# Performance work log

Hardware: AMD Instinct MI355X
Metric: run time of the kernel (lower is better)

## Reference

```python
import jax, jax.numpy as jnp
import numpy as np

H = 12          # num attention heads
D_HEAD = 64     # head size (768 / 12)
P = 2           # power-law exponent
C = 5.0         # score shift
EPS = 1e-10


def setup_inputs() -> dict:
    key = jax.random.key(0)
    ks = jax.random.split(key, 8)
    B, S, Dm = 32, 512, 768
    scale = 1.0 / np.sqrt(Dm)
    return {
        "hidden_states": jax.random.normal(ks[0], (B, S, Dm), dtype=jnp.float32),
        "attention_mask": jnp.ones((B, 1, 1, S), dtype=jnp.float32),
        "Wq": jax.random.normal(ks[1], (Dm, Dm), dtype=jnp.float32) * scale,
        "bq": jnp.zeros((Dm,), dtype=jnp.float32),
        "Wk": jax.random.normal(ks[2], (Dm, Dm), dtype=jnp.float32) * scale,
        "bk": jnp.zeros((Dm,), dtype=jnp.float32),
        "Wv": jax.random.normal(ks[3], (Dm, Dm), dtype=jnp.float32) * scale,
        "bv": jnp.zeros((Dm,), dtype=jnp.float32),
    }


def _heads(x, B, S):
    # [B, S, H*d] -> [B, H, S, d]
    return x.reshape(B, S, H, D_HEAD).transpose(0, 2, 1, 3)


def reference(hidden_states, attention_mask, Wq, bq, Wk, bk, Wv, bv):
    B, S, Dm = hidden_states.shape
    q = _heads(hidden_states @ Wq + bq, B, S)
    k = _heads(hidden_states @ Wk + bk, B, S)
    v = _heads(hidden_states @ Wv + bv, B, S)

    inv_sqrt_d = 1.0 / (np.sqrt(D_HEAD) + 1e-10)
    scores = jnp.einsum("bhqd,bhkd->bhqk", q, k) * inv_sqrt_d  # [B,H,S,S]

    # Power-law attention (Powerformer, distill=0 branch)
    probs = jnp.power(scores + C, P)
    probs = probs / (jnp.sum(probs, axis=-1, keepdims=True) + EPS)
    probs = probs * attention_mask  # mask multiplied after normalization

    ctx = jnp.einsum("bhqk,bhkd->bhqd", probs, v)  # [B,H,S,d]
    ctx = ctx.transpose(0, 2, 1, 3).reshape(B, S, Dm)
    return ctx
```

## Files before the change

kernel.cpp:

```cpp
#include <hip/hip_runtime.h>

typedef __attribute__((ext_vector_type(8))) _Float16 half8;
typedef __attribute__((ext_vector_type(4))) _Float16 half4;
typedef __attribute__((ext_vector_type(4))) float f32x4;

#define MFMA_K32(a, b, c) __builtin_amdgcn_mfma_f32_16x16x32_f16((a), (b), (c), 0, 0, 0)
#define MFMA_K16(a, b, c) __builtin_amdgcn_mfma_f32_16x16x16f16((a), (b), (c), 0, 0, 0)

__device__ inline void async16(const _Float16* g, _Float16* l) {
    __builtin_amdgcn_global_load_lds(
        (const __attribute__((address_space(1))) void*)g,
        (__attribute__((address_space(3))) void*)l, 16, 0, 0);
}


__global__ __launch_bounds__(256) void prep_kernel(
    const float* __restrict__ X, _Float16* __restrict__ Xh,
    const float* __restrict__ W0, const float* __restrict__ W1,
    const float* __restrict__ W2,
    _Float16* __restrict__ T0, _Float16* __restrict__ T1,
    _Float16* __restrict__ T2)
{
    __shared__ float tile[32][33];
    int bid = blockIdx.x;
    if (bid < 6144) {
        size_t idx = ((size_t)bid * 256 + threadIdx.x) * 8;
        float4 a = *(const float4*)(X + idx);
        float4 c = *(const float4*)(X + idx + 4);
        half8 hv;
        hv[0] = (_Float16)a.x; hv[1] = (_Float16)a.y;
        hv[2] = (_Float16)a.z; hv[3] = (_Float16)a.w;
        hv[4] = (_Float16)c.x; hv[5] = (_Float16)c.y;
        hv[6] = (_Float16)c.z; hv[7] = (_Float16)c.w;
        *(half8*)(Xh + idx) = hv;
    } else {
        int id = bid - 6144;
        int z = id / 576; id -= z * 576;
        int n0 = (id / 24) * 32, k0 = (id % 24) * 32;
        const float* W = (z == 0) ? W0 : (z == 1) ? W1 : W2;
        _Float16* T = (z == 0) ? T0 : (z == 1) ? T1 : T2;
        int tx = threadIdx.x & 31, ty = threadIdx.x >> 5;
#pragma unroll
        for (int r = 0; r < 4; ++r)
            tile[ty + 8 * r][tx] = W[(size_t)(k0 + ty + 8 * r) * 768 + n0 + tx];
        __syncthreads();
#pragma unroll
        for (int r = 0; r < 4; ++r)
            T[(size_t)(n0 + ty + 8 * r) * 768 + k0 + tx] =
                (_Float16)tile[tx][ty + 8 * r];
    }
}

__global__ __launch_bounds__(256) void qkv_gemm(
    const _Float16* __restrict__ Xh,
    const _Float16* __restrict__ W0, const _Float16* __restrict__ W1,
    const _Float16* __restrict__ W2,
    const float* __restrict__ b0, const float* __restrict__ b1,
    const float* __restrict__ b2,
    const float* __restrict__ mask,
    _Float16* __restrict__ Qo, _Float16* __restrict__ Ko,
    _Float16* __restrict__ Vo)
{
    int z = blockIdx.y / 6;
    int n0 = (blockIdx.y % 6) * 128;
    int m0 = blockIdx.x * 128;
    const _Float16* Wt = (z == 0) ? W0 : (z == 1) ? W1 : W2;
    const float* bias = (z == 0) ? b0 : (z == 1) ? b1 : b2;

    __shared__ __attribute__((aligned(16))) _Float16 As[2 * 8192];
    __shared__ __attribute__((aligned(16))) _Float16 Bs[2 * 8192];

    int t = threadIdx.x;
    int wave = t >> 6, lane = t & 63, quad = lane >> 4, l16 = lane & 15;
    int wm = (wave & 1) * 64, wn = (wave >> 1) * 64;

    int srow = t >> 3;
    int sg = (t & 7) ^ (srow & 7);

    const _Float16* gA = Xh + (size_t)(m0 + srow) * 768 + sg * 8;
    const _Float16* gB = Wt + (size_t)(n0 + srow) * 768 + sg * 8;
    _Float16* lA = As + t * 8;
    _Float16* lB = Bs + t * 8;

#define STAGE(buf, k0v) do {                                                   \
        async16(gA,                    lA + (buf) * 8192);                     \
        async16(gA + (size_t)1 * 32 * 768 + (k0v) - (k0v) + (k0v), lA + (buf) * 8192 + 2048); \
        async16(gA + (size_t)2 * 32 * 768 + (k0v), lA + (buf) * 8192 + 4096);  \
        async16(gA + (size_t)3 * 32 * 768 + (k0v), lA + (buf) * 8192 + 6144);  \
        async16(gB + (k0v),            lB + (buf) * 8192);                     \
        async16(gB + (size_t)1 * 32 * 768 + (k0v), lB + (buf) * 8192 + 2048);  \
        async16(gB + (size_t)2 * 32 * 768 + (k0v), lB + (buf) * 8192 + 4096);  \
        async16(gB + (size_t)3 * 32 * 768 + (k0v), lB + (buf) * 8192 + 6144); } while (0)
#undef STAGE
#define STAGE(buf, k0v) do {                                                   \
        async16(gA + (k0v),                        lA + (buf) * 8192);         \
        async16(gA + (size_t)1 * 32 * 768 + (k0v), lA + (buf) * 8192 + 2048);  \
        async16(gA + (size_t)2 * 32 * 768 + (k0v), lA + (buf) * 8192 + 4096);  \
        async16(gA + (size_t)3 * 32 * 768 + (k0v), lA + (buf) * 8192 + 6144);  \
        async16(gB + (k0v),                        lB + (buf) * 8192);         \
        async16(gB + (size_t)1 * 32 * 768 + (k0v), lB + (buf) * 8192 + 2048);  \
        async16(gB + (size_t)2 * 32 * 768 + (k0v), lB + (buf) * 8192 + 4096);  \
        async16(gB + (size_t)3 * 32 * 768 + (k0v), lB + (buf) * 8192 + 6144); } while (0)

    const _Float16* Pa = (z == 2) ? As : Bs;
    const _Float16* Pb = (z == 2) ? Bs : As;

    f32x4 acc[4][4] = {};

    STAGE(0, 0);

    for (int kt = 0; kt < 12; ++kt) {
        int c = kt & 1;
        if (kt < 11) {
            STAGE(c ^ 1, (kt + 1) * 64);
            asm volatile("s_waitcnt vmcnt(8)" ::: "memory");
        } else {
            asm volatile("s_waitcnt vmcnt(0)" ::: "memory");
        }
        __builtin_amdgcn_s_barrier();
        __builtin_amdgcn_sched_barrier(0);

        const _Float16* Pa_ = Pa + c * 8192;
        const _Float16* Pb_ = Pb + c * 8192;
#pragma unroll
        for (int ks = 0; ks < 2; ++ks) {
            half8 af[4], bf[4];
#pragma unroll
            for (int i = 0; i < 4; ++i) {
                int row = wm + i * 16 + l16;
                af[i] = *(const half8*)&Pa_[row * 64 +
                                            (((ks << 2) + quad) ^ (row & 7)) * 8];
            }
#pragma unroll
            for (int j = 0; j < 4; ++j) {
                int row = wn + j * 16 + l16;
                bf[j] = *(const half8*)&Pb_[row * 64 +
                                            (((ks << 2) + quad) ^ (row & 7)) * 8];
            }
#pragma unroll
            for (int i = 0; i < 4; ++i)
#pragma unroll
                for (int j = 0; j < 4; ++j)
                    acc[i][j] = MFMA_K32(af[i], bf[j], acc[i][j]);
        }
        __builtin_amdgcn_sched_barrier(0);
        __builtin_amdgcn_s_barrier();
    }
#undef STAGE

    if (z != 2) {
#pragma unroll
        for (int i = 0; i < 4; ++i) {
            int nbase = n0 + wm + i * 16 + quad * 4;
            int hh = nbase >> 6, dbase = nbase & 63;
            float4 bv4 = *(const float4*)&bias[nbase];
#pragma unroll
            for (int j = 0; j < 4; ++j) {
                int token = m0 + wn + j * 16 + l16;
                int bb = token >> 9, s = token & 511;
                half4 pk;
                if (z == 0) {
#pragma unroll
                    for (int r = 0; r < 4; ++r)
                        pk[r] = (_Float16)((acc[i][j][r] + ((const float*)&bv4)[r]) * 0.125f);
                } else {
#pragma unroll
                    for (int r = 0; r < 4; ++r)
                        pk[r] = (_Float16)(acc[i][j][r] + ((const float*)&bv4)[r]);
                }
                size_t off = (((size_t)(bb * 12 + hh)) * 512 + s) * 64 + dbase;
                if (z == 0) *(half4*)&Qo[off] = pk;
                else        *(half4*)&Ko[off] = pk;
            }
        }
    } else {
        float mk[4][4];
#pragma unroll
        for (int i = 0; i < 4; ++i) {
            int mbase = m0 + wm + i * 16 + quad * 4;
            int bb = mbase >> 9, s = mbase & 511;
#pragma unroll
            for (int r = 0; r < 4; ++r)
                mk[i][r] = mask[(size_t)bb * 512 + s + r];
        }
#pragma unroll
        for (int j = 0; j < 4; ++j) {
            int n = n0 + wn + j * 16 + l16;
            float bv = bias[n];
            int hh = n >> 6, d = n & 63;
#pragma unroll
            for (int i = 0; i < 4; ++i) {
                int mbase = m0 + wm + i * 16 + quad * 4;
                int bb = mbase >> 9, s = mbase & 511;
                half4 pk;
#pragma unroll
                for (int r = 0; r < 4; ++r)
                    pk[r] = (_Float16)((acc[i][j][r] + bv) * mk[i][r]);
                size_t off = (((size_t)(bb * 12 + hh)) * 64 + d) * 512 + s;
                *(half4*)&Vo[off] = pk;
            }
        }
    }
}

__global__ __launch_bounds__(256) void attn_kernel(
    const _Float16* __restrict__ Q, const _Float16* __restrict__ K,
    const _Float16* __restrict__ Vt, float* __restrict__ out)
{
    __shared__ __attribute__((aligned(16))) _Float16 Ks[2][64 * 88];
    __shared__ __attribute__((aligned(16))) _Float16 Vs[2][64 * 88];

    int t = threadIdx.x;
    int wave = t >> 6, lane = t & 63, quad = lane >> 4, l16 = lane & 15;
    int h = blockIdx.y, b = blockIdx.z;
    size_t bh = (size_t)b * 12 + h;
    const _Float16* Qp = Q + bh * (512 * 64);
    const _Float16* Kp = K + bh * (512 * 64);
    const _Float16* Vp = Vt + bh * (64 * 512);
    int qbase = blockIdx.x * 256 + wave * 64;

    half8 qf[4][2];
#pragma unroll
    for (int i = 0; i < 4; ++i)
#pragma unroll
        for (int ks = 0; ks < 2; ++ks)
            qf[i][ks] = *(const half8*)(Qp + (size_t)(qbase + i * 16 + l16) * 64 +
                                        ks * 32 + quad * 8);

    f32x4 ctx[4][4] = {};
    f32x4 rsum[4] = {};
    const half4 ones = {(_Float16)1.f, (_Float16)1.f, (_Float16)1.f, (_Float16)1.f};

    int srow = t >> 2, spart = (t & 3) * 16;
    const _Float16* kgb = Kp + (size_t)srow * 64 + spart;
    const _Float16* vgb = Vp + (size_t)srow * 512 + spart;

    half8 ka0 = *(const half8*)(kgb);
    half8 ka1 = *(const half8*)(kgb + 8);
    half8 va0 = *(const half8*)(vgb);
    half8 va1 = *(const half8*)(vgb + 8);
    *(half8*)&Ks[0][srow * 88 + spart] = ka0;
    *(half8*)&Ks[0][srow * 88 + spart + 8] = ka1;
    *(half8*)&Vs[0][srow * 88 + spart] = va0;
    *(half8*)&Vs[0][srow * 88 + spart + 8] = va1;
    __syncthreads();

    for (int kt = 0; kt < 8; ++kt) {
        int c = kt & 1;
        if (kt < 7) {
            size_t ko = (size_t)(kt + 1) * 64;
            ka0 = *(const half8*)(kgb + ko * 64);
            ka1 = *(const half8*)(kgb + ko * 64 + 8);
            va0 = *(const half8*)(vgb + ko);
            va1 = *(const half8*)(vgb + ko + 8);
        }

        __builtin_amdgcn_s_setprio(1);
#pragma unroll
        for (int kb = 0; kb < 4; ++kb) {
            half8 kf0 = *(const half8*)&Ks[c][(kb * 16 + l16) * 88 + quad * 8];
            half8 kf1 = *(const half8*)&Ks[c][(kb * 16 + l16) * 88 + 32 + quad * 8];
            f32x4 sc[4];
#pragma unroll
            for (int i = 0; i < 4; ++i) {
                f32x4 s0 = {0.f, 0.f, 0.f, 0.f};
                s0 = MFMA_K32(kf0, qf[i][0], s0);
                sc[i] = MFMA_K32(kf1, qf[i][1], s0);
            }
            half4 pA[4];
#pragma unroll
            for (int i = 0; i < 4; ++i) {
#pragma unroll
                for (int r = 0; r < 4; ++r) {
                    float s = sc[i][r] + 5.0f;
                    pA[i][r] = (_Float16)(s * s);
                }
            }
#pragma unroll
            for (int i = 0; i < 4; ++i)
                rsum[i] = MFMA_K16(pA[i], ones, rsum[i]);
#pragma unroll
            for (int n = 0; n < 4; ++n) {
                half4 vf = *(const half4*)&Vs[c][(n * 16 + l16) * 88 + kb * 16 + quad * 4];
#pragma unroll
                for (int i = 0; i < 4; ++i)
                    ctx[i][n] = MFMA_K16(pA[i], vf, ctx[i][n]);
            }
        }
        __builtin_amdgcn_s_setprio(0);

        if (kt < 7) {
            *(half8*)&Ks[1 - c][srow * 88 + spart] = ka0;
            *(half8*)&Ks[1 - c][srow * 88 + spart + 8] = ka1;
            *(half8*)&Vs[1 - c][srow * 88 + spart] = va0;
            *(half8*)&Vs[1 - c][srow * 88 + spart + 8] = va1;
        }
        __syncthreads();
    }

#pragma unroll
    for (int i = 0; i < 4; ++i) {
        f32x4 inv;
#pragma unroll
        for (int r = 0; r < 4; ++r)
            inv[r] = 1.0f / (rsum[i][r] + 1e-10f);
#pragma unroll
        for (int n = 0; n < 4; ++n)
#pragma unroll
            for (int r = 0; r < 4; ++r) {
                int q = qbase + i * 16 + quad * 4 + r;
                int d = n * 16 + l16;
                out[((size_t)b * 512 + q) * 768 + h * 64 + d] =
                    ctx[i][n][r] * inv[r];
            }
    }
}

extern "C" void kernel_launch(void* const* d_in, const int* in_sizes, int n_in,
                              void* d_out, int out_size, void* d_ws, size_t ws_size,
                              hipStream_t stream)
{
    const float* hs   = (const float*)d_in[0];
    const float* mask = (const float*)d_in[1];
    const float* Wq   = (const float*)d_in[2];
    const float* bq   = (const float*)d_in[3];
    const float* Wk   = (const float*)d_in[4];
    const float* bk   = (const float*)d_in[5];
    const float* Wv   = (const float*)d_in[6];
    const float* bv   = (const float*)d_in[7];
    float* out = (float*)d_out;

    char* ws = (char*)d_ws;
    _Float16* Wtq = (_Float16*)ws;
    _Float16* Wtk = Wtq + 768 * 768;
    _Float16* Wtv = Wtk + 768 * 768;
    _Float16* Qb  = Wtv + 768 * 768;
    _Float16* Kb  = Qb + 16384 * 768;
    _Float16* Vb  = Kb + 16384 * 768;
    _Float16* Xh = (_Float16*)d_out;

    prep_kernel<<<dim3(7872), 256, 0, stream>>>(hs, Xh, Wq, Wk, Wv,
                                                Wtq, Wtk, Wtv);
    qkv_gemm<<<dim3(128, 18), 256, 0, stream>>>(Xh, Wtq, Wtk, Wtv,
                                                bq, bk, bv, mask, Qb, Kb, Vb);
    attn_kernel<<<dim3(2, 12, 32), 256, 0, stream>>>(Qb, Kb, Vb, out);
}
```

Baseline: 239.5 us.

## Fuse fp32-to-fp16 activation cast into QKV GEMM A-tile loads

Removes the separate pass that converted hidden_states to fp16 in global memory. The QKV GEMM now loads fp32 activation tiles into registers, converts them, and writes fp16 into LDS, prefetching one k-step ahead. The fp16 weight transpose/cast kernel remains. The change avoids a full write and re-read of the fp16 activation copy. In exchange each GEMM block reads twice the A bytes from global memory, and the 18 column blocks that share a row tile each redo the same conversion. It also adds register pressure and synchronous LDS stores in place of async global-to-LDS copies.

```diff
diff --git a/kernel.cpp b/kernel.cpp
--- a/kernel.cpp
+++ b/kernel.cpp
@@ -14,45 +14,30 @@
 }
 
 
-__global__ __launch_bounds__(256) void prep_kernel(
-    const float* __restrict__ X, _Float16* __restrict__ Xh,
+__global__ __launch_bounds__(256) void wcast_kernel(
     const float* __restrict__ W0, const float* __restrict__ W1,
     const float* __restrict__ W2,
     _Float16* __restrict__ T0, _Float16* __restrict__ T1,
     _Float16* __restrict__ T2)
 {
+    int z = blockIdx.z;
+    const float* W = (z == 0) ? W0 : (z == 1) ? W1 : W2;
+    _Float16* T = (z == 0) ? T0 : (z == 1) ? T1 : T2;
     __shared__ float tile[32][33];
-    int bid = blockIdx.x;
-    if (bid < 6144) {
-        size_t idx = ((size_t)bid * 256 + threadIdx.x) * 8;
-        float4 a = *(const float4*)(X + idx);
-        float4 c = *(const float4*)(X + idx + 4);
-        half8 hv;
-        hv[0] = (_Float16)a.x; hv[1] = (_Float16)a.y;
-        hv[2] = (_Float16)a.z; hv[3] = (_Float16)a.w;
-        hv[4] = (_Float16)c.x; hv[5] = (_Float16)c.y;
-        hv[6] = (_Float16)c.z; hv[7] = (_Float16)c.w;
-        *(half8*)(Xh + idx) = hv;
-    } else {
-        int id = bid - 6144;
-        int z = id / 576; id -= z * 576;
-        int n0 = (id / 24) * 32, k0 = (id % 24) * 32;
-        const float* W = (z == 0) ? W0 : (z == 1) ? W1 : W2;
-        _Float16* T = (z == 0) ? T0 : (z == 1) ? T1 : T2;
-        int tx = threadIdx.x & 31, ty = threadIdx.x >> 5;
-#pragma unroll
-        for (int r = 0; r < 4; ++r)
-            tile[ty + 8 * r][tx] = W[(size_t)(k0 + ty + 8 * r) * 768 + n0 + tx];
-        __syncthreads();
-#pragma unroll
-        for (int r = 0; r < 4; ++r)
-            T[(size_t)(n0 + ty + 8 * r) * 768 + k0 + tx] =
-                (_Float16)tile[tx][ty + 8 * r];
-    }
+    int n0 = blockIdx.x * 32, k0 = blockIdx.y * 32;
+    int tx = threadIdx.x & 31, ty = threadIdx.x >> 5;
+#pragma unroll
+    for (int r = 0; r < 4; ++r)
+        tile[ty + 8 * r][tx] = W[(size_t)(k0 + ty + 8 * r) * 768 + n0 + tx];
+    __syncthreads();
+#pragma unroll
+    for (int r = 0; r < 4; ++r)
+        T[(size_t)(n0 + ty + 8 * r) * 768 + k0 + tx] =
+            (_Float16)tile[tx][ty + 8 * r];
 }
 
 __global__ __launch_bounds__(256) void qkv_gemm(
-    const _Float16* __restrict__ Xh,
+    const float* __restrict__ X,
     const _Float16* __restrict__ W0, const _Float16* __restrict__ W1,
     const _Float16* __restrict__ W2,
     const float* __restrict__ b0, const float* __restrict__ b1,
@@ -77,43 +62,52 @@
     int srow = t >> 3;
     int sg = (t & 7) ^ (srow & 7);
 
-    const _Float16* gA = Xh + (size_t)(m0 + srow) * 768 + sg * 8;
+    const float*    gX = X  + (size_t)(m0 + srow) * 768 + sg * 8;
     const _Float16* gB = Wt + (size_t)(n0 + srow) * 768 + sg * 8;
     _Float16* lA = As + t * 8;
     _Float16* lB = Bs + t * 8;
 
-#define STAGE(buf, k0v) do {                                                   \
-        async16(gA,                    lA + (buf) * 8192);                     \
-        async16(gA + (size_t)1 * 32 * 768 + (k0v) - (k0v) + (k0v), lA + (buf) * 8192 + 2048); \
-        async16(gA + (size_t)2 * 32 * 768 + (k0v), lA + (buf) * 8192 + 4096);  \
-        async16(gA + (size_t)3 * 32 * 768 + (k0v), lA + (buf) * 8192 + 6144);  \
-        async16(gB + (k0v),            lB + (buf) * 8192);                     \
-        async16(gB + (size_t)1 * 32 * 768 + (k0v), lB + (buf) * 8192 + 2048);  \
-        async16(gB + (size_t)2 * 32 * 768 + (k0v), lB + (buf) * 8192 + 4096);  \
-        async16(gB + (size_t)3 * 32 * 768 + (k0v), lB + (buf) * 8192 + 6144); } while (0)
-#undef STAGE
-#define STAGE(buf, k0v) do {                                                   \
-        async16(gA + (k0v),                        lA + (buf) * 8192);         \
-        async16(gA + (size_t)1 * 32 * 768 + (k0v), lA + (buf) * 8192 + 2048);  \
-        async16(gA + (size_t)2 * 32 * 768 + (k0v), lA + (buf) * 8192 + 4096);  \
-        async16(gA + (size_t)3 * 32 * 768 + (k0v), lA + (buf) * 8192 + 6144);  \
+#define STAGE_B(buf, k0v) do {                                                 \
         async16(gB + (k0v),                        lB + (buf) * 8192);         \
         async16(gB + (size_t)1 * 32 * 768 + (k0v), lB + (buf) * 8192 + 2048);  \
         async16(gB + (size_t)2 * 32 * 768 + (k0v), lB + (buf) * 8192 + 4096);  \
         async16(gB + (size_t)3 * 32 * 768 + (k0v), lB + (buf) * 8192 + 6144); } while (0)
 
+#define LOAD_A(k0v) do {                                                       \
+        _Pragma("unroll")                                                      \
+        for (int q = 0; q < 4; ++q) {                                          \
+            const float* p = gX + (size_t)q * 32 * 768 + (k0v);                \
+            a4[q][0] = *(const float4*)p;                                      \
+            a4[q][1] = *(const float4*)(p + 4);                                \
+        } } while (0)
+
+#define WRITE_A(buf) do {                                                      \
+        _Pragma("unroll")                                                      \
+        for (int q = 0; q < 4; ++q) {                                          \
+            half8 hv;                                                          \
+            hv[0] = (_Float16)a4[q][0].x; hv[1] = (_Float16)a4[q][0].y;        \
+            hv[2] = (_Float16)a4[q][0].z; hv[3] = (_Float16)a4[q][0].w;        \
+            hv[4] = (_Float16)a4[q][1].x; hv[5] = (_Float16)a4[q][1].y;        \
+            hv[6] = (_Float16)a4[q][1].z; hv[7] = (_Float16)a4[q][1].w;        \
+            *(half8*)(lA + (buf) * 8192 + q * 2048) = hv;                      \
+        } } while (0)
+
     const _Float16* Pa = (z == 2) ? As : Bs;
     const _Float16* Pb = (z == 2) ? Bs : As;
 
+    float4 a4[4][2];
     f32x4 acc[4][4] = {};
 
-    STAGE(0, 0);
+    STAGE_B(0, 0);
+    LOAD_A(0);
 
     for (int kt = 0; kt < 12; ++kt) {
         int c = kt & 1;
+        if (kt < 11) STAGE_B(c ^ 1, (kt + 1) * 64);
+        WRITE_A(c);
         if (kt < 11) {
-            STAGE(c ^ 1, (kt + 1) * 64);
-            asm volatile("s_waitcnt vmcnt(8)" ::: "memory");
+            LOAD_A((kt + 1) * 64);
+            asm volatile("s_waitcnt vmcnt(12)" ::: "memory");
         } else {
             asm volatile("s_waitcnt vmcnt(0)" ::: "memory");
         }
@@ -146,7 +140,9 @@
         __builtin_amdgcn_sched_barrier(0);
         __builtin_amdgcn_s_barrier();
     }
-#undef STAGE
+#undef STAGE_B
+#undef LOAD_A
+#undef WRITE_A
 
     if (z != 2) {
 #pragma unroll
@@ -337,11 +333,10 @@
     _Float16* Qb  = Wtv + 768 * 768;
     _Float16* Kb  = Qb + 16384 * 768;
     _Float16* Vb  = Kb + 16384 * 768;
-    _Float16* Xh = (_Float16*)d_out;
-
-    prep_kernel<<<dim3(7872), 256, 0, stream>>>(hs, Xh, Wq, Wk, Wv,
-                                                Wtq, Wtk, Wtv);
-    qkv_gemm<<<dim3(128, 18), 256, 0, stream>>>(Xh, Wtq, Wtk, Wtv,
+
+    wcast_kernel<<<dim3(24, 24, 3), 256, 0, stream>>>(Wq, Wk, Wv,
+                                                      Wtq, Wtk, Wtv);
+    qkv_gemm<<<dim3(128, 18), 256, 0, stream>>>(hs, Wtq, Wtk, Wtv,
                                                 bq, bk, bv, mask, Qb, Kb, Vb);
     attn_kernel<<<dim3(2, 12, 32), 256, 0, stream>>>(Qb, Kb, Vb, out);
 }
```

After: 253.1 us. 5.7% more time.
